# Optimization experiments

Measured on AMD Instinct MI355X. Metric: run time of the kernel, lower is better.

## Reference

```python
import jax, jax.numpy as jnp
import numpy as np


def setup_inputs() -> dict:
    key = jax.random.key(0)
    N, C, E, S = 200000, 128, 3200000, 5000
    k0, k1, k2 = jax.random.split(key, 3)
    x = jax.random.normal(k0, (N, C), dtype=jnp.float32)
    edge_index = jax.random.randint(k1, (2, E), 0, N, dtype=jnp.int32)
    starts = (jnp.arange(S, dtype=jnp.int32) * (N // S))  # sorted sentence start offsets
    node1_indices = starts
    node2_indices = starts + 1
    sent_indices = starts + 2
    W = jax.random.normal(k2, (C, 1), dtype=jnp.float32) * 0.1
    b = jnp.zeros((1,), dtype=jnp.float32)
    return dict(x=x, edge_index=edge_index, node1_indices=node1_indices,
                node2_indices=node2_indices, sent_indices=sent_indices,
                W=W, b=b, alpha=4)


def _gcn_score(x, edge_index, W, b):
    # PyG GCNConv: h = xW; add self-loops; sym-normalized aggregation; + bias
    N = x.shape[0]
    h = x @ W  # [N, 1]
    row, col = edge_index[0], edge_index[1]
    ones = jnp.ones(row.shape[0], dtype=x.dtype)
    deg = jax.ops.segment_sum(ones, col, num_segments=N) + 1.0  # self-loop included
    dis = jax.lax.rsqrt(deg)
    norm = dis[row] * dis[col]
    agg = jax.ops.segment_sum(h[row] * norm[:, None], col, num_segments=N)
    out = agg + h * (dis * dis)[:, None]  # self-loop term, norm = 1/deg
    return (out + b).squeeze(-1)  # [N]


def reference(x, edge_index, node1_indices, node2_indices, sent_indices, W, b, alpha):
    N = x.shape[0]
    S = node1_indices.shape[0]
    score = _gcn_score(x, edge_index, W, b)  # [N]

    # per-sentence segment ids: segment i = [node1_indices[i], node1_indices[i+1])
    seg = jnp.searchsorted(node1_indices, jnp.arange(N, dtype=node1_indices.dtype), side='right') - 1
    seg = jnp.clip(seg, 0, S - 1)

    # numerically-stable per-segment softmax of scores
    m = jax.ops.segment_max(score, seg, num_segments=S)
    e = jnp.exp(score - m[seg])
    Z = jax.ops.segment_sum(e, seg, num_segments=S)
    p = e / Z[seg]  # normalized scores per sentence

    # cutoff = max(p) - alpha * std(p) per sentence (population std, as np.std)
    cnt = jax.ops.segment_sum(jnp.ones(N, dtype=p.dtype), seg, num_segments=S)
    pmax = jax.ops.segment_max(p, seg, num_segments=S)
    mean = jax.ops.segment_sum(p, seg, num_segments=S) / cnt
    var = jax.ops.segment_sum(p * p, seg, num_segments=S) / cnt - mean * mean
    std = jnp.sqrt(jnp.maximum(var, 0.0))
    cutoff = pmax - jnp.float32(alpha) * std
    keep = p >= cutoff[seg]

    # union with node1/node2/sent special nodes (always kept)
    keep = keep.at[node1_indices].set(True)
    keep = keep.at[node2_indices].set(True)
    keep = keep.at[sent_indices].set(True)

    # remap: position of each kept node in the compacted ordering
    pos = jnp.cumsum(keep.astype(jnp.int32)) - 1  # valid only where keep

    # gated node features (masked-dense form of x[perm] * tanh(score[perm]))
    x_out = jnp.where(keep[:, None], x * jnp.tanh(score)[:, None], 0.0)

    new_node1 = pos[node1_indices]
    new_node2 = pos[node2_indices]
    new_sent = pos[sent_indices]

    # filter_adj: keep edges with both endpoints kept, remap endpoints
    row, col = edge_index[0], edge_index[1]
    edge_keep = keep[row] & keep[col]
    new_edge_index = jnp.where(edge_keep[None, :], pos[edge_index], -1)

    return (x_out, new_edge_index, keep, edge_keep, new_node1, new_node2, new_sent)
```

## Files before the change

### kernel.cpp

```cpp
#include <hip/hip_runtime.h>
#include <math.h>

#define WAVE 64
#define FXSCALE 4398046511104.0
#define WINDOW 7936
#define NBMAX 32
#define BINB 2048

typedef float vfloat4 __attribute__((ext_vector_type(4)));

__global__ void k_h_hist(const float* __restrict__ x, const float* __restrict__ W,
                         double* __restrict__ h,
                         const int* __restrict__ ecol, int* __restrict__ binCnt,
                         int N, int C, int E, int NB, int nhb) {
    int b = blockIdx.x;
    if (b < nhb) {
        int t = b * 256 + threadIdx.x;
        int row = t >> 5;
        int lane = t & 31;
        if (row >= N) return;
        const float4* xr = (const float4*)(x + (size_t)row * C);
        const float4* w4 = (const float4*)W;
        int C4 = C >> 2;
        double acc = 0.0;
        for (int c = lane; c < C4; c += 32) {
            float4 xv = xr[c];
            float4 wv = w4[c];
            acc += (double)xv.x * (double)wv.x + (double)xv.y * (double)wv.y
                 + (double)xv.z * (double)wv.z + (double)xv.w * (double)wv.w;
        }
        #pragma unroll
        for (int o = 16; o > 0; o >>= 1) acc += __shfl_xor(acc, o);
        if (lane == 0) h[row] = acc;
    } else {
        __shared__ int cnt[NBMAX];
        int tid = threadIdx.x;
        if (tid < NBMAX) cnt[tid] = 0;
        __syncthreads();
        int hb = b - nhb;
        for (long e = (long)hb * 256 + tid; e < E; e += 512L * 256)
            atomicAdd(&cnt[ecol[e] / WINDOW], 1);
        __syncthreads();
        if (tid < NB && cnt[tid] > 0) atomicAdd(&binCnt[tid], cnt[tid]);
    }
}

__global__ void k_off(const int* __restrict__ binCnt, int* __restrict__ binOff,
                      int* __restrict__ binWr, int NB) {
    if (threadIdx.x != 0 || blockIdx.x != 0) return;
    int acc = 0;
    for (int i = 0; i < NB; i++) {
        binOff[i] = acc;
        binWr[i] = acc;
        acc += binCnt[i];
    }
    binOff[NB] = acc;
}

__global__ void k_bin(const int* __restrict__ erow, const int* __restrict__ ecol,
                      int* __restrict__ binWr, int* __restrict__ binnedRow,
                      unsigned short* __restrict__ binnedCol16, int E, int NB) {
    __shared__ int cnt[NBMAX];
    __shared__ int lbase[NBMAX];
    __shared__ int gbase[NBMAX];
    __shared__ int lrow[BINB];
    __shared__ unsigned short lcol[BINB];
    __shared__ unsigned char lbin[BINB];
    int tid = threadIdx.x;
    if (tid < NBMAX) cnt[tid] = 0;
    __syncthreads();
    long b0 = (long)blockIdx.x * BINB;
    int n = (int)((E - b0) < (long)BINB ? (E - b0) : (long)BINB);
    int bA[8], rkA[8], rwA[8];
    unsigned short clA[8];
    #pragma unroll
    for (int k = 0; k < 8; k++) bA[k] = -1;
    int base_i = tid * 8;
    if (base_i + 8 <= n) {
        long e = b0 + base_i;
        int4 r0 = *(const int4*)(erow + e), r1 = *(const int4*)(erow + e + 4);
        int4 c0 = *(const int4*)(ecol + e), c1 = *(const int4*)(ecol + e + 4);
        int rr[8] = {r0.x, r0.y, r0.z, r0.w, r1.x, r1.y, r1.z, r1.w};
        int cc[8] = {c0.x, c0.y, c0.z, c0.w, c1.x, c1.y, c1.z, c1.w};
        #pragma unroll
        for (int k = 0; k < 8; k++) {
            int c = cc[k];
            int bb = c / WINDOW;
            bA[k] = bb; rwA[k] = rr[k]; clA[k] = (unsigned short)(c - bb * WINDOW);
            rkA[k] = atomicAdd(&cnt[bb], 1);
        }
    } else {
        for (int k = 0; k < 8; k++) {
            int i = base_i + k;
            if (i < n) {
                long e = b0 + i;
                int c = ecol[e];
                int bb = c / WINDOW;
                bA[k] = bb; rwA[k] = erow[e]; clA[k] = (unsigned short)(c - bb * WINDOW);
                rkA[k] = atomicAdd(&cnt[bb], 1);
            }
        }
    }
    __syncthreads();
    if (tid == 0) {
        int acc = 0;
        for (int i = 0; i < NB; i++) { lbase[i] = acc; acc += cnt[i]; }
    }
    __syncthreads();
    if (tid < NB && cnt[tid] > 0) gbase[tid] = atomicAdd(&binWr[tid], cnt[tid]);
    __syncthreads();
    #pragma unroll
    for (int k = 0; k < 8; k++) {
        if (bA[k] >= 0) {
            int l = lbase[bA[k]] + rkA[k];
            lrow[l] = rwA[k];
            lcol[l] = clA[k];
            lbin[l] = (unsigned char)bA[k];
        }
    }
    __syncthreads();
    for (int l = tid; l < n; l += 256) {
        int bb = lbin[l];
        int g = gbase[bb] + (l - lbase[bb]);
        binnedRow[g] = lrow[l];
        binnedCol16[g] = lcol[l];
    }
}

__global__ void k_degb(const unsigned short* __restrict__ binnedCol16,
                       const int* __restrict__ binOff,
                       unsigned int* __restrict__ partialDeg, int N, int Md) {
    __shared__ unsigned int cnt[WINDOW];
    int bin = blockIdx.x / Md, m = blockIdx.x % Md;
    int tid = threadIdx.x;
    for (int i = tid; i < WINDOW; i += blockDim.x) cnt[i] = 0;
    __syncthreads();
    int st = binOff[bin], en = binOff[bin + 1];
    for (int idx = st + m * (int)blockDim.x + tid; idx < en; idx += Md * (int)blockDim.x)
        atomicAdd(&cnt[binnedCol16[idx]], 1u);
    __syncthreads();
    int wb = bin * WINDOW;
    for (int i = tid; i < WINDOW && wb + i < N; i += blockDim.x)
        partialDeg[(size_t)m * N + wb + i] = cnt[i];
}

__global__ void k_dis_hd(const unsigned int* __restrict__ partialDeg,
                         const double* __restrict__ h,
                         double* __restrict__ dis, double* __restrict__ hd,
                         int N, int Md) {
    int i = blockIdx.x * blockDim.x + threadIdx.x;
    if (i >= N) return;
    unsigned int dsum = 0;
    for (int m = 0; m < Md; m++) dsum += partialDeg[(size_t)m * N + i];
    double d = 1.0 / sqrt((double)dsum + 1.0);
    dis[i] = d;
    hd[i] = h[i] * d;
}

__global__ void k_aggb(const int* __restrict__ binnedRow,
                       const unsigned short* __restrict__ binnedCol16,
                       const int* __restrict__ binOff,
                       const double* __restrict__ hd, const double* __restrict__ dis,
                       unsigned long long* __restrict__ partialAgg, int N, int Ma) {
    __shared__ unsigned long long acc[WINDOW];
    int bin = blockIdx.x / Ma, m = blockIdx.x % Ma;
    int tid = threadIdx.x;
    for (int i = tid; i < WINDOW; i += blockDim.x) acc[i] = 0ULL;
    __syncthreads();
    int st = binOff[bin], en = binOff[bin + 1];
    int wb = bin * WINDOW;
    for (int idx = st + m * (int)blockDim.x + tid; idx < en; idx += Ma * (int)blockDim.x) {
        int r = binnedRow[idx];
        int c16 = binnedCol16[idx];
        long long q = __double2ll_rn(hd[r] * dis[wb + c16] * FXSCALE);
        atomicAdd(&acc[c16], (unsigned long long)q);
    }
    __syncthreads();
    for (int i = tid; i < WINDOW && wb + i < N; i += blockDim.x)
        partialAgg[(size_t)m * N + wb + i] = acc[i];
}

__global__ void k_score(const unsigned long long* __restrict__ partialAgg,
                        const double* __restrict__ h, const double* __restrict__ dis,
                        const float* __restrict__ bptr,
                        float* __restrict__ score32, float* __restrict__ tg,
                        int N, int Ma) {
    int i = blockIdx.x * blockDim.x + threadIdx.x;
    if (i >= N) return;
    long long acc = 0;
    for (int m = 0; m < Ma; m++) acc += (long long)partialAgg[(size_t)m * N + i];
    double agg = (double)acc / FXSCALE;
    double d = dis[i];
    double sc = (agg + h[i] * (d * d)) + (double)bptr[0];
    score32[i] = (float)sc;
    tg[i] = (float)tanh(sc);
}

__global__ void k_seg_np(const float* __restrict__ score32, const int* __restrict__ starts,
                         float* __restrict__ p32, int* __restrict__ keepI,
                         const int* __restrict__ alphaPtr,
                         const int* __restrict__ n1, const int* __restrict__ n2,
                         const int* __restrict__ sent, int N, int S) {
    int g = blockIdx.x * blockDim.x + threadIdx.x;
    if (g >= S) return;
    int st = starts[g];
    int en = (g == S - 1) ? N : starts[g + 1];
    if (en <= st) return;

    int ai = alphaPtr[0];
    float alpha = (ai >= 0 && ai < 1000000) ? (float)ai : __int_as_float(ai);

    float m = -3.402823466e38f;
    for (int i = st; i < en; i++) m = fmaxf(m, score32[i]);

    float Z = 0.0f;
    for (int i = st; i < en; i++) {
        float dm = __fsub_rn(score32[i], m);
        float e = (float)exp((double)dm);
        p32[i] = e;
        Z = __fadd_rn(Z, e);
    }

    float sp = 0.0f, sq = 0.0f, pm = -3.402823466e38f;
    for (int i = st; i < en; i++) {
        float p = __fdiv_rn(p32[i], Z);
        p32[i] = p;
        sp = __fadd_rn(sp, p);
        sq = __fadd_rn(sq, __fmul_rn(p, p));
        pm = fmaxf(pm, p);
    }

    float cnt_ = (float)(en - st);
    float mean = __fdiv_rn(sp, cnt_);
    float var = __fsub_rn(__fdiv_rn(sq, cnt_), __fmul_rn(mean, mean));
    float sd = sqrtf(fmaxf(var, 0.0f));
    float cutoff = __fsub_rn(pm, __fmul_rn(alpha, sd));

    for (int i = st; i < en; i++) keepI[i] = (p32[i] >= cutoff) ? 1 : 0;

    keepI[n1[g]] = 1;
    keepI[n2[g]] = 1;
    keepI[sent[g]] = 1;
}

#define SCAN_CHUNK 2048

__global__ void k_scanA(const int* __restrict__ keepI, int* __restrict__ bs, int N) {
    int tid = threadIdx.x;
    long base = (long)blockIdx.x * SCAN_CHUNK + (long)tid * 8;
    int s = 0;
    #pragma unroll
    for (int k = 0; k < 8; k++) { long i = base + k; if (i < N) s += keepI[i]; }
    __shared__ int sm[256];
    sm[tid] = s; __syncthreads();
    for (int off = 128; off > 0; off >>= 1) {
        if (tid < off) sm[tid] += sm[tid + off];
        __syncthreads();
    }
    if (tid == 0) bs[blockIdx.x] = sm[0];
}

__global__ void k_scanB(const int* __restrict__ bs, int* __restrict__ bo, int nb) {
    __shared__ int sm[256];
    __shared__ int carrySh;
    int tid = threadIdx.x;
    if (tid == 0) carrySh = 0;
    __syncthreads();
    for (int base = 0; base < nb; base += 256) {
        int i = base + tid;
        int v = (i < nb) ? bs[i] : 0;
        sm[tid] = v; __syncthreads();
        for (int off = 1; off < 256; off <<= 1) {
            int t = (tid >= off) ? sm[tid - off] : 0;
            __syncthreads();
            sm[tid] += t;
            __syncthreads();
        }
        int incl = sm[tid];
        int total = sm[255];
        int carry = carrySh;
        if (i < nb) bo[i] = carry + incl - v;
        __syncthreads();
        if (tid == 0) carrySh = carry + total;
        __syncthreads();
    }
}

__global__ void k_scanC(const int* __restrict__ keepI, const int* __restrict__ bo,
                        const float* __restrict__ tg,
                        float* __restrict__ posF, float* __restrict__ gate,
                        float* __restrict__ o_keep, int N) {
    int tid = threadIdx.x;
    long base = (long)blockIdx.x * SCAN_CHUNK + (long)tid * 8;
    int v[8];
    int th = 0;
    #pragma unroll
    for (int k = 0; k < 8; k++) {
        long i = base + k;
        v[k] = (i < N) ? keepI[i] : 0;
        th += v[k];
    }
    __shared__ int sm[256];
    sm[tid] = th; __syncthreads();
    for (int off = 1; off < 256; off <<= 1) {
        int t = (tid >= off) ? sm[tid - off] : 0;
        __syncthreads();
        sm[tid] += t;
        __syncthreads();
    }
    int excl = sm[tid] - th;
    int run = bo[blockIdx.x] + excl;
    #pragma unroll
    for (int k = 0; k < 8; k++) {
        long i = base + k;
        if (i < N) {
            posF[i] = v[k] ? (float)(run + v[k] - 1) : -1.0f;
            gate[i] = v[k] ? tg[i] : 0.0f;
            o_keep[i] = v[k] ? 1.0f : 0.0f;
            run += v[k];
        }
    }
}

__global__ void k_out(const float4* __restrict__ x4, const float* __restrict__ gate,
                      float* __restrict__ o_x, long total4,
                      const int* __restrict__ erow, const int* __restrict__ ecol,
                      const float* __restrict__ posF,
                      float* __restrict__ o_edge, float* __restrict__ o_ekeep, int E,
                      const int* __restrict__ n1, const int* __restrict__ n2,
                      const int* __restrict__ sent,
                      float* __restrict__ o_n1, float* __restrict__ o_n2,
                      float* __restrict__ o_sent, int S,
                      int nxb, int neb4) {
    int b = blockIdx.x;
    if (b < nxb) {
        long idx = (long)b * blockDim.x + threadIdx.x;
        if (idx >= total4) return;
        int row = (int)(idx >> 5);
        float g = gate[row];
        float4 v = x4[idx];
        vfloat4 r = { v.x * g, v.y * g, v.z * g, v.w * g };
        __builtin_nontemporal_store(r, (vfloat4*)o_x + idx);
    } else if (b < nxb + neb4) {
        long e0 = ((long)(b - nxb) * blockDim.x + threadIdx.x) * 4;
        if (e0 >= E) return;
        if (e0 + 3 < E) {
            int4 r4 = *(const int4*)(erow + e0);
            int4 c4 = *(const int4*)(ecol + e0);
            vfloat4 oer, oec, ok;
            #pragma unroll
            for (int k = 0; k < 4; k++) {
                int r = (&r4.x)[k], c = (&c4.x)[k];
                float pr = posF[r], pc = posF[c];
                bool ek = (pr >= 0.0f) && (pc >= 0.0f);
                oer[k] = ek ? pr : -1.0f;
                oec[k] = ek ? pc : -1.0f;
                ok[k]  = ek ? 1.0f : 0.0f;
            }
            __builtin_nontemporal_store(oer, (vfloat4*)(o_edge + e0));
            __builtin_nontemporal_store(oec, (vfloat4*)(o_edge + (size_t)E + e0));
            __builtin_nontemporal_store(ok,  (vfloat4*)(o_ekeep + e0));
        } else {
            for (long e = e0; e < E; e++) {
                int r = erow[e], c = ecol[e];
                float pr = posF[r], pc = posF[c];
                bool ek = (pr >= 0.0f) && (pc >= 0.0f);
                o_edge[e] = ek ? pr : -1.0f;
                o_edge[(size_t)E + e] = ek ? pc : -1.0f;
                o_ekeep[e] = ek ? 1.0f : 0.0f;
            }
        }
    } else {
        int i = (b - nxb - neb4) * blockDim.x + threadIdx.x;
        if (i >= S) return;
        o_n1[i] = posF[n1[i]];
        o_n2[i] = posF[n2[i]];
        o_sent[i] = posF[sent[i]];
    }
}

extern "C" void kernel_launch(void* const* d_in, const int* in_sizes, int n_in,
                              void* d_out, int out_size, void* d_ws, size_t ws_size,
                              hipStream_t stream) {
    const float* x    = (const float*)d_in[0];
    const int*   eidx = (const int*)d_in[1];
    const int*   n1   = (const int*)d_in[2];
    const int*   n2   = (const int*)d_in[3];
    const int*   sent = (const int*)d_in[4];
    const float* W    = (const float*)d_in[5];
    const float* bp   = (const float*)d_in[6];
    const int*   alphaPtr = (const int*)d_in[7];

    int C = in_sizes[5];
    int N = in_sizes[0] / C;
    int E = in_sizes[1] / 2;
    int S = in_sizes[2];

    const int* erow = eidx;
    const int* ecol = eidx + E;

    int NB = (N + WINDOW - 1) / WINDOW;
    const int Md = 8, Ma = 8;

    char* ws = (char*)d_ws;
    size_t off = 0;
    auto alloc = [&](size_t bytes) { void* p = ws + off; off += (bytes + 255) & ~(size_t)255; return p; };
    int*   binCnt = (int*)  alloc(NBMAX * 4);
    int*   binOff = (int*)  alloc((NBMAX + 1) * 4);
    int*   binWr  = (int*)  alloc(NBMAX * 4);
    int*   binnedRow = (int*)alloc((size_t)E * 4);
    unsigned short* binnedCol16 = (unsigned short*)alloc((size_t)E * 2);
    unsigned int* partialDeg = (unsigned int*)alloc((size_t)Md * N * 4);
    unsigned long long* partialAgg = (unsigned long long*)alloc((size_t)Ma * N * 8);
    double* h     = (double*)alloc((size_t)N * 8);
    double* dis   = (double*)alloc((size_t)N * 8);
    double* hd    = (double*)alloc((size_t)N * 8);
    float* score32 = (float*)alloc((size_t)N * 4);
    float* p32    = (float*)alloc((size_t)N * 4);
    float* tg     = (float*)alloc((size_t)N * 4);
    int*   keepI  = (int*)  alloc((size_t)N * 4);
    float* posF   = (float*)alloc((size_t)N * 4);
    float* gate   = (float*)alloc((size_t)N * 4);
    int nb = (N + SCAN_CHUNK - 1) / SCAN_CHUNK;
    int*   bs     = (int*)  alloc((size_t)nb * 4);
    int*   bo     = (int*)  alloc((size_t)nb * 4);

    float* o_x     = (float*)d_out;
    float* o_edge  = o_x + (size_t)N * C;
    float* o_keep  = o_edge + 2 * (size_t)E;
    float* o_ekeep = o_keep + N;
    float* o_n1    = o_ekeep + E;
    float* o_n2    = o_n1 + S;
    float* o_sent  = o_n2 + S;

    (void)hipMemsetAsync(binCnt, 0, NBMAX * 4, stream);

    int nhb = (N * 32 + 255) / 256;
    k_h_hist<<<nhb + 512, 256, 0, stream>>>(x, W, h, ecol, binCnt, N, C, E, NB, nhb);
    k_off<<<1, 64, 0, stream>>>(binCnt, binOff, binWr, NB);
    int nBatches = (int)(((long)E + BINB - 1) / BINB);
    k_bin<<<nBatches, 256, 0, stream>>>(erow, ecol, binWr, binnedRow, binnedCol16, E, NB);
    k_degb<<<NB * Md, 256, 0, stream>>>(binnedCol16, binOff, partialDeg, N, Md);
    k_dis_hd<<<(N + 255) / 256, 256, 0, stream>>>(partialDeg, h, dis, hd, N, Md);
    k_aggb<<<NB * Ma, 256, 0, stream>>>(binnedRow, binnedCol16, binOff, hd, dis, partialAgg, N, Ma);
    k_score<<<(N + 255) / 256, 256, 0, stream>>>(partialAgg, h, dis, bp, score32, tg, N, Ma);
    k_seg_np<<<(S + 255) / 256, 256, 0, stream>>>(score32, n1, p32, keepI, alphaPtr, n1, n2, sent, N, S);
    k_scanA<<<nb, 256, 0, stream>>>(keepI, bs, N);
    k_scanB<<<1, 256, 0, stream>>>(bs, bo, nb);
    k_scanC<<<nb, 256, 0, stream>>>(keepI, bo, tg, posF, gate, o_keep, N);

    long total4 = (long)N * (C / 4);
    int nxb = (int)((total4 + 255) / 256);
    long e4 = (E + 3) / 4;
    int neb4 = (int)((e4 + 255) / 256);
    int nsb = (S + 255) / 256;
    k_out<<<nxb + neb4 + nsb, 256, 0, stream>>>(
        (const float4*)x, gate, o_x, total4,
        erow, ecol, posF, o_edge, o_ekeep, E,
        n1, n2, sent, o_n1, o_n2, o_sent, S, nxb, neb4);
}
```

Baseline: 251.6 us.

## Fuse small pipeline kernels via last-block reductions and decoupled-lookback scan

```diff
diff --git a/kernel.cpp b/kernel.cpp
--- a/kernel.cpp
+++ b/kernel.cpp
@@ -1,11 +1,11 @@
 #include <hip/hip_runtime.h>
 #include <math.h>
 
-#define WAVE 64
 #define FXSCALE 4398046511104.0
 #define WINDOW 7936
 #define NBMAX 32
 #define BINB 2048
+#define SCAN_CHUNK 2048
 
 typedef float vfloat4 __attribute__((ext_vector_type(4)));
 
@@ -45,24 +45,14 @@
     }
 }
 
-__global__ void k_off(const int* __restrict__ binCnt, int* __restrict__ binOff,
-                      int* __restrict__ binWr, int NB) {
-    if (threadIdx.x != 0 || blockIdx.x != 0) return;
-    int acc = 0;
-    for (int i = 0; i < NB; i++) {
-        binOff[i] = acc;
-        binWr[i] = acc;
-        acc += binCnt[i];
-    }
-    binOff[NB] = acc;
-}
-
 __global__ void k_bin(const int* __restrict__ erow, const int* __restrict__ ecol,
-                      int* __restrict__ binWr, int* __restrict__ binnedRow,
+                      const int* __restrict__ binCnt, int* __restrict__ binWr0,
+                      int* __restrict__ binnedRow,
                       unsigned short* __restrict__ binnedCol16, int E, int NB) {
     __shared__ int cnt[NBMAX];
     __shared__ int lbase[NBMAX];
     __shared__ int gbase[NBMAX];
+    __shared__ int boff[NBMAX];
     __shared__ int lrow[BINB];
     __shared__ unsigned short lcol[BINB];
     __shared__ unsigned char lbin[BINB];
@@ -105,9 +95,12 @@
     if (tid == 0) {
         int acc = 0;
         for (int i = 0; i < NB; i++) { lbase[i] = acc; acc += cnt[i]; }
-    }
-    __syncthreads();
-    if (tid < NB && cnt[tid] > 0) gbase[tid] = atomicAdd(&binWr[tid], cnt[tid]);
+        int acc2 = 0;
+        for (int i = 0; i < NB; i++) { boff[i] = acc2; acc2 += binCnt[i]; }
+    }
+    __syncthreads();
+    if (tid < NB && cnt[tid] > 0)
+        gbase[tid] = boff[tid] + atomicAdd(&binWr0[tid], cnt[tid]);
     __syncthreads();
     #pragma unroll
     for (int k = 0; k < 8; k++) {
@@ -128,72 +121,92 @@
 }
 
 __global__ void k_degb(const unsigned short* __restrict__ binnedCol16,
-                       const int* __restrict__ binOff,
-                       unsigned int* __restrict__ partialDeg, int N, int Md) {
+                       const int* __restrict__ binCnt,
+                       unsigned int* __restrict__ partialDeg, int* __restrict__ doneD,
+                       const double* __restrict__ h,
+                       double* __restrict__ dis, double* __restrict__ hd,
+                       int N, int Md, int NB) {
     __shared__ unsigned int cnt[WINDOW];
+    __shared__ int boff[NBMAX + 1];
+    __shared__ int lastFlag;
     int bin = blockIdx.x / Md, m = blockIdx.x % Md;
     int tid = threadIdx.x;
-    for (int i = tid; i < WINDOW; i += blockDim.x) cnt[i] = 0;
-    __syncthreads();
-    int st = binOff[bin], en = binOff[bin + 1];
-    for (int idx = st + m * (int)blockDim.x + tid; idx < en; idx += Md * (int)blockDim.x)
+    if (tid == 0) {
+        int acc = 0;
+        for (int i = 0; i < NB; i++) { boff[i] = acc; acc += binCnt[i]; }
+        boff[NB] = acc;
+    }
+    for (int i = tid; i < WINDOW; i += 256) cnt[i] = 0;
+    __syncthreads();
+    int st = boff[bin], en = boff[bin + 1];
+    for (int idx = st + m * 256 + tid; idx < en; idx += Md * 256)
         atomicAdd(&cnt[binnedCol16[idx]], 1u);
     __syncthreads();
     int wb = bin * WINDOW;
-    for (int i = tid; i < WINDOW && wb + i < N; i += blockDim.x)
+    int wlim = (N - wb) < WINDOW ? (N - wb) : WINDOW;
+    for (int i = tid; i < wlim; i += 256)
         partialDeg[(size_t)m * N + wb + i] = cnt[i];
-}
-
-__global__ void k_dis_hd(const unsigned int* __restrict__ partialDeg,
-                         const double* __restrict__ h,
-                         double* __restrict__ dis, double* __restrict__ hd,
-                         int N, int Md) {
-    int i = blockIdx.x * blockDim.x + threadIdx.x;
-    if (i >= N) return;
-    unsigned int dsum = 0;
-    for (int m = 0; m < Md; m++) dsum += partialDeg[(size_t)m * N + i];
-    double d = 1.0 / sqrt((double)dsum + 1.0);
-    dis[i] = d;
-    hd[i] = h[i] * d;
+    __threadfence();
+    if (tid == 0) lastFlag = (atomicAdd(&doneD[bin], 1) == Md - 1) ? 1 : 0;
+    __syncthreads();
+    if (!lastFlag) return;
+    __threadfence();
+    for (int i = tid; i < wlim; i += 256) {
+        unsigned int d = 0;
+        for (int mm = 0; mm < Md; mm++) d += partialDeg[(size_t)mm * N + wb + i];
+        double dd = 1.0 / sqrt((double)d + 1.0);
+        dis[wb + i] = dd;
+        hd[wb + i] = h[wb + i] * dd;
+    }
 }
 
 __global__ void k_aggb(const int* __restrict__ binnedRow,
                        const unsigned short* __restrict__ binnedCol16,
-                       const int* __restrict__ binOff,
+                       const int* __restrict__ binCnt,
                        const double* __restrict__ hd, const double* __restrict__ dis,
-                       unsigned long long* __restrict__ partialAgg, int N, int Ma) {
+                       const double* __restrict__ h, const float* __restrict__ bptr,
+                       unsigned long long* __restrict__ partialAgg, int* __restrict__ doneA,
+                       float* __restrict__ score32, float* __restrict__ tg,
+                       int N, int Ma, int NB) {
     __shared__ unsigned long long acc[WINDOW];
+    __shared__ int boff[NBMAX + 1];
+    __shared__ int lastFlag;
     int bin = blockIdx.x / Ma, m = blockIdx.x % Ma;
     int tid = threadIdx.x;
-    for (int i = tid; i < WINDOW; i += blockDim.x) acc[i] = 0ULL;
-    __syncthreads();
-    int st = binOff[bin], en = binOff[bin + 1];
+    if (tid == 0) {
+        int a = 0;
+        for (int i = 0; i < NB; i++) { boff[i] = a; a += binCnt[i]; }
+        boff[NB] = a;
+    }
+    for (int i = tid; i < WINDOW; i += 256) acc[i] = 0ULL;
+    __syncthreads();
+    int st = boff[bin], en = boff[bin + 1];
     int wb = bin * WINDOW;
-    for (int idx = st + m * (int)blockDim.x + tid; idx < en; idx += Ma * (int)blockDim.x) {
+    for (int idx = st + m * 256 + tid; idx < en; idx += Ma * 256) {
         int r = binnedRow[idx];
         int c16 = binnedCol16[idx];
         long long q = __double2ll_rn(hd[r] * dis[wb + c16] * FXSCALE);
         atomicAdd(&acc[c16], (unsigned long long)q);
     }
     __syncthreads();
-    for (int i = tid; i < WINDOW && wb + i < N; i += blockDim.x)
+    int wlim = (N - wb) < WINDOW ? (N - wb) : WINDOW;
+    for (int i = tid; i < wlim; i += 256)
         partialAgg[(size_t)m * N + wb + i] = acc[i];
-}
-
-__global__ void k_score(const unsigned long long* __restrict__ partialAgg,
-                        const double* __restrict__ h, const double* __restrict__ dis,
-                        const float* __restrict__ bptr,
-                        float* __restrict__ score32, float* __restrict__ tg,
-                        int N, int Ma) {
-    int i = blockIdx.x * blockDim.x + threadIdx.x;
-    if (i >= N) return;
-    long long acc = 0;
-    for (int m = 0; m < Ma; m++) acc += (long long)partialAgg[(size_t)m * N + i];
-    double agg = (double)acc / FXSCALE;
-    double d = dis[i];
-    double sc = (agg + h[i] * (d * d)) + (double)bptr[0];
-    score32[i] = (float)sc;
-    tg[i] = (float)tanh(sc);
+    __threadfence();
+    if (tid == 0) lastFlag = (atomicAdd(&doneA[bin], 1) == Ma - 1) ? 1 : 0;
+    __syncthreads();
+    if (!lastFlag) return;
+    __threadfence();
+    double bb = (double)bptr[0];
+    for (int i = tid; i < wlim; i += 256) {
+        long long a = 0;
+        for (int mm = 0; mm < Ma; mm++) a += (long long)partialAgg[(size_t)mm * N + wb + i];
+        double agg = (double)a / FXSCALE;
+        double d = dis[wb + i];
+        double sc = (agg + h[wb + i] * (d * d)) + bb;
+        score32[wb + i] = (float)sc;
+        tg[wb + i] = (float)tanh(sc);
+    }
 }
 
 __global__ void k_seg_np(const float* __restrict__ score32, const int* __restrict__ starts,
@@ -243,55 +256,13 @@
     keepI[sent[g]] = 1;
 }
 
-#define SCAN_CHUNK 2048
-
-__global__ void k_scanA(const int* __restrict__ keepI, int* __restrict__ bs, int N) {
+__global__ void k_scan(const int* __restrict__ keepI, const float* __restrict__ tg,
+                       unsigned long long* __restrict__ stArr,
+                       float* __restrict__ posF, float* __restrict__ gate,
+                       float* __restrict__ o_keep, int N) {
     int tid = threadIdx.x;
-    long base = (long)blockIdx.x * SCAN_CHUNK + (long)tid * 8;
-    int s = 0;
-    #pragma unroll
-    for (int k = 0; k < 8; k++) { long i = base + k; if (i < N) s += keepI[i]; }
-    __shared__ int sm[256];
-    sm[tid] = s; __syncthreads();
-    for (int off = 128; off > 0; off >>= 1) {
-        if (tid < off) sm[tid] += sm[tid + off];
-        __syncthreads();
-    }
-    if (tid == 0) bs[blockIdx.x] = sm[0];
-}
-
-__global__ void k_scanB(const int* __restrict__ bs, int* __restrict__ bo, int nb) {
-    __shared__ int sm[256];
-    __shared__ int carrySh;
-    int tid = threadIdx.x;
-    if (tid == 0) carrySh = 0;
-    __syncthreads();
-    for (int base = 0; base < nb; base += 256) {
-        int i = base + tid;
-        int v = (i < nb) ? bs[i] : 0;
-        sm[tid] = v; __syncthreads();
-        for (int off = 1; off < 256; off <<= 1) {
-            int t = (tid >= off) ? sm[tid - off] : 0;
-            __syncthreads();
-            sm[tid] += t;
-            __syncthreads();
-        }
-        int incl = sm[tid];
-        int total = sm[255];
-        int carry = carrySh;
-        if (i < nb) bo[i] = carry + incl - v;
-        __syncthreads();
-        if (tid == 0) carrySh = carry + total;
-        __syncthreads();
-    }
-}
-
-__global__ void k_scanC(const int* __restrict__ keepI, const int* __restrict__ bo,
-                        const float* __restrict__ tg,
-                        float* __restrict__ posF, float* __restrict__ gate,
-                        float* __restrict__ o_keep, int N) {
-    int tid = threadIdx.x;
-    long base = (long)blockIdx.x * SCAN_CHUNK + (long)tid * 8;
+    int b = blockIdx.x;
+    long base = (long)b * SCAN_CHUNK + (long)tid * 8;
     int v[8];
     int th = 0;
     #pragma unroll
@@ -308,8 +279,30 @@
         sm[tid] += t;
         __syncthreads();
     }
-    int excl = sm[tid] - th;
-    int run = bo[blockIdx.x] + excl;
+    int total = sm[255];
+    __shared__ int exclSh;
+    if (tid == 0) {
+        if (b == 0) {
+            atomicExch(&stArr[0], (2ULL << 62) | (unsigned long long)(unsigned)total);
+            exclSh = 0;
+        } else {
+            atomicExch(&stArr[b], (1ULL << 62) | (unsigned long long)(unsigned)total);
+            int excl = 0;
+            int j = b - 1;
+            while (true) {
+                unsigned long long s = atomicAdd(&stArr[j], 0ULL);
+                unsigned state = (unsigned)(s >> 62);
+                if (state == 0) continue;
+                excl += (int)(s & 0x3FFFFFFFFFFFFFFFULL);
+                if (state == 2u) break;
+                j--;
+            }
+            atomicExch(&stArr[b], (2ULL << 62) | (unsigned long long)(unsigned)(excl + total));
+            exclSh = excl;
+        }
+    }
+    __syncthreads();
+    int run = exclSh + sm[tid] - th;
     #pragma unroll
     for (int k = 0; k < 8; k++) {
         long i = base + k;
@@ -406,8 +399,11 @@
     size_t off = 0;
     auto alloc = [&](size_t bytes) { void* p = ws + off; off += (bytes + 255) & ~(size_t)255; return p; };
     int*   binCnt = (int*)  alloc(NBMAX * 4);
-    int*   binOff = (int*)  alloc((NBMAX + 1) * 4);
-    int*   binWr  = (int*)  alloc(NBMAX * 4);
+    int*   binWr0 = (int*)  alloc(NBMAX * 4);
+    int*   doneD  = (int*)  alloc(NBMAX * 4);
+    int*   doneA  = (int*)  alloc(NBMAX * 4);
+    unsigned long long* scanSt = (unsigned long long*)alloc(256 * 8);
+    size_t zeroBytes = (size_t)((char*)(scanSt + 256) - (char*)binCnt);
     int*   binnedRow = (int*)alloc((size_t)E * 4);
     unsigned short* binnedCol16 = (unsigned short*)alloc((size_t)E * 2);
     unsigned int* partialDeg = (unsigned int*)alloc((size_t)Md * N * 4);
@@ -421,9 +417,6 @@
     int*   keepI  = (int*)  alloc((size_t)N * 4);
     float* posF   = (float*)alloc((size_t)N * 4);
     float* gate   = (float*)alloc((size_t)N * 4);
-    int nb = (N + SCAN_CHUNK - 1) / SCAN_CHUNK;
-    int*   bs     = (int*)  alloc((size_t)nb * 4);
-    int*   bo     = (int*)  alloc((size_t)nb * 4);
 
     float* o_x     = (float*)d_out;
     float* o_edge  = o_x + (size_t)N * C;
@@ -433,21 +426,18 @@
     float* o_n2    = o_n1 + S;
     float* o_sent  = o_n2 + S;
 
-    (void)hipMemsetAsync(binCnt, 0, NBMAX * 4, stream);
+    (void)hipMemsetAsync(binCnt, 0, zeroBytes, stream);
 
     int nhb = (N * 32 + 255) / 256;
     k_h_hist<<<nhb + 512, 256, 0, stream>>>(x, W, h, ecol, binCnt, N, C, E, NB, nhb);
-    k_off<<<1, 64, 0, stream>>>(binCnt, binOff, binWr, NB);
     int nBatches = (int)(((long)E + BINB - 1) / BINB);
-    k_bin<<<nBatches, 256, 0, stream>>>(erow, ecol, binWr, binnedRow, binnedCol16, E, NB);
-    k_degb<<<NB * Md, 256, 0, stream>>>(binnedCol16, binOff, partialDeg, N, Md);
-    k_dis_hd<<<(N + 255) / 256, 256, 0, stream>>>(partialDeg, h, dis, hd, N, Md);
-    k_aggb<<<NB * Ma, 256, 0, stream>>>(binnedRow, binnedCol16, binOff, hd, dis, partialAgg, N, Ma);
-    k_score<<<(N + 255) / 256, 256, 0, stream>>>(partialAgg, h, dis, bp, score32, tg, N, Ma);
+    k_bin<<<nBatches, 256, 0, stream>>>(erow, ecol, binCnt, binWr0, binnedRow, binnedCol16, E, NB);
+    k_degb<<<NB * Md, 256, 0, stream>>>(binnedCol16, binCnt, partialDeg, doneD, h, dis, hd, N, Md, NB);
+    k_aggb<<<NB * Ma, 256, 0, stream>>>(binnedRow, binnedCol16, binCnt, hd, dis, h, bp,
+                                        partialAgg, doneA, score32, tg, N, Ma, NB);
     k_seg_np<<<(S + 255) / 256, 256, 0, stream>>>(score32, n1, p32, keepI, alphaPtr, n1, n2, sent, N, S);
-    k_scanA<<<nb, 256, 0, stream>>>(keepI, bs, N);
-    k_scanB<<<1, 256, 0, stream>>>(bs, bo, nb);
-    k_scanC<<<nb, 256, 0, stream>>>(keepI, bo, tg, posF, gate, o_keep, N);
+    int nb = (N + SCAN_CHUNK - 1) / SCAN_CHUNK;
+    k_scan<<<nb, 256, 0, stream>>>(keepI, tg, scanSt, posF, gate, o_keep, N);
 
     long total4 = (long)N * (C / 4);
     int nxb = (int)((total4 + 255) / 256);
```

Result: slower. 444.6 us (+76.7%).

## Replace three-kernel scan with single-pass decoupled look-back scan

Applied to the files above, without the earlier changes.

```diff
diff --git a/kernel.cpp b/kernel.cpp
--- a/kernel.cpp
+++ b/kernel.cpp
@@ -1,11 +1,11 @@
 #include <hip/hip_runtime.h>
 #include <math.h>
 
-#define WAVE 64
 #define FXSCALE 4398046511104.0
 #define WINDOW 7936
 #define NBMAX 32
 #define BINB 2048
+#define SCAN_CHUNK 2048
 
 typedef float vfloat4 __attribute__((ext_vector_type(4)));
 
@@ -243,55 +243,13 @@
     keepI[sent[g]] = 1;
 }
 
-#define SCAN_CHUNK 2048
-
-__global__ void k_scanA(const int* __restrict__ keepI, int* __restrict__ bs, int N) {
+__global__ void k_scan(const int* __restrict__ keepI, const float* __restrict__ tg,
+                       unsigned long long* __restrict__ stArr,
+                       float* __restrict__ posF, float* __restrict__ gate,
+                       float* __restrict__ o_keep, int N) {
     int tid = threadIdx.x;
-    long base = (long)blockIdx.x * SCAN_CHUNK + (long)tid * 8;
-    int s = 0;
-    #pragma unroll
-    for (int k = 0; k < 8; k++) { long i = base + k; if (i < N) s += keepI[i]; }
-    __shared__ int sm[256];
-    sm[tid] = s; __syncthreads();
-    for (int off = 128; off > 0; off >>= 1) {
-        if (tid < off) sm[tid] += sm[tid + off];
-        __syncthreads();
-    }
-    if (tid == 0) bs[blockIdx.x] = sm[0];
-}
-
-__global__ void k_scanB(const int* __restrict__ bs, int* __restrict__ bo, int nb) {
-    __shared__ int sm[256];
-    __shared__ int carrySh;
-    int tid = threadIdx.x;
-    if (tid == 0) carrySh = 0;
-    __syncthreads();
-    for (int base = 0; base < nb; base += 256) {
-        int i = base + tid;
-        int v = (i < nb) ? bs[i] : 0;
-        sm[tid] = v; __syncthreads();
-        for (int off = 1; off < 256; off <<= 1) {
-            int t = (tid >= off) ? sm[tid - off] : 0;
-            __syncthreads();
-            sm[tid] += t;
-            __syncthreads();
-        }
-        int incl = sm[tid];
-        int total = sm[255];
-        int carry = carrySh;
-        if (i < nb) bo[i] = carry + incl - v;
-        __syncthreads();
-        if (tid == 0) carrySh = carry + total;
-        __syncthreads();
-    }
-}
-
-__global__ void k_scanC(const int* __restrict__ keepI, const int* __restrict__ bo,
-                        const float* __restrict__ tg,
-                        float* __restrict__ posF, float* __restrict__ gate,
-                        float* __restrict__ o_keep, int N) {
-    int tid = threadIdx.x;
-    long base = (long)blockIdx.x * SCAN_CHUNK + (long)tid * 8;
+    int b = blockIdx.x;
+    long base = (long)b * SCAN_CHUNK + (long)tid * 8;
     int v[8];
     int th = 0;
     #pragma unroll
@@ -308,8 +266,30 @@
         sm[tid] += t;
         __syncthreads();
     }
-    int excl = sm[tid] - th;
-    int run = bo[blockIdx.x] + excl;
+    int total = sm[255];
+    __shared__ int exclSh;
+    if (tid == 0) {
+        if (b == 0) {
+            atomicExch(&stArr[0], (2ULL << 62) | (unsigned long long)(unsigned)total);
+            exclSh = 0;
+        } else {
+            atomicExch(&stArr[b], (1ULL << 62) | (unsigned long long)(unsigned)total);
+            int excl = 0;
+            int j = b - 1;
+            while (true) {
+                unsigned long long s = atomicAdd(&stArr[j], 0ULL);
+                unsigned state = (unsigned)(s >> 62);
+                if (state == 0) continue;
+                excl += (int)(s & 0x3FFFFFFFFFFFFFFFULL);
+                if (state == 2u) break;
+                j--;
+            }
+            atomicExch(&stArr[b], (2ULL << 62) | (unsigned long long)(unsigned)(excl + total));
+            exclSh = excl;
+        }
+    }
+    __syncthreads();
+    int run = exclSh + sm[tid] - th;
     #pragma unroll
     for (int k = 0; k < 8; k++) {
         long i = base + k;
@@ -406,6 +386,8 @@
     size_t off = 0;
     auto alloc = [&](size_t bytes) { void* p = ws + off; off += (bytes + 255) & ~(size_t)255; return p; };
     int*   binCnt = (int*)  alloc(NBMAX * 4);
+    unsigned long long* scanSt = (unsigned long long*)alloc(256 * 8);
+    size_t zeroBytes = (size_t)((char*)(scanSt + 256) - (char*)binCnt);
     int*   binOff = (int*)  alloc((NBMAX + 1) * 4);
     int*   binWr  = (int*)  alloc(NBMAX * 4);
     int*   binnedRow = (int*)alloc((size_t)E * 4);
@@ -421,9 +403,6 @@
     int*   keepI  = (int*)  alloc((size_t)N * 4);
     float* posF   = (float*)alloc((size_t)N * 4);
     float* gate   = (float*)alloc((size_t)N * 4);
-    int nb = (N + SCAN_CHUNK - 1) / SCAN_CHUNK;
-    int*   bs     = (int*)  alloc((size_t)nb * 4);
-    int*   bo     = (int*)  alloc((size_t)nb * 4);
 
     float* o_x     = (float*)d_out;
     float* o_edge  = o_x + (size_t)N * C;
@@ -433,7 +412,7 @@
     float* o_n2    = o_n1 + S;
     float* o_sent  = o_n2 + S;
 
-    (void)hipMemsetAsync(binCnt, 0, NBMAX * 4, stream);
+    (void)hipMemsetAsync(binCnt, 0, zeroBytes, stream);
 
     int nhb = (N * 32 + 255) / 256;
     k_h_hist<<<nhb + 512, 256, 0, stream>>>(x, W, h, ecol, binCnt, N, C, E, NB, nhb);
@@ -445,9 +424,8 @@
     k_aggb<<<NB * Ma, 256, 0, stream>>>(binnedRow, binnedCol16, binOff, hd, dis, partialAgg, N, Ma);
     k_score<<<(N + 255) / 256, 256, 0, stream>>>(partialAgg, h, dis, bp, score32, tg, N, Ma);
     k_seg_np<<<(S + 255) / 256, 256, 0, stream>>>(score32, n1, p32, keepI, alphaPtr, n1, n2, sent, N, S);
-    k_scanA<<<nb, 256, 0, stream>>>(keepI, bs, N);
-    k_scanB<<<1, 256, 0, stream>>>(bs, bo, nb);
-    k_scanC<<<nb, 256, 0, stream>>>(keepI, bo, tg, posF, gate, o_keep, N);
+    int nb = (N + SCAN_CHUNK - 1) / SCAN_CHUNK;
+    k_scan<<<nb, 256, 0, stream>>>(keepI, tg, scanSt, posF, gate, o_keep, N);
 
     long total4 = (long)N * (C / 4);
     int nxb = (int)((total4 + 255) / 256);
```

After: 252.4 us. No clear change (+0.3%).
